# Kernel tuning notes

Hardware: AMD Instinct MI355X
Metric: run time of the kernel (lower is better)

Reference implementation:

```python
import jax, jax.numpy as jnp
import numpy as np

N_IN = 500000
C = 64
K = 27          # kernel volume 3^3
P = 150000      # max pairs per kernel offset
NUM_OUT = 200000


def setup_inputs() -> dict:
    key = jax.random.key(0)
    k1, k2, k3 = jax.random.split(key, 3)
    features = jax.random.normal(k1, (N_IN, C), dtype=jnp.float32)
    # indice_pairs[k, 0, :] = input voxel indices, indice_pairs[k, 1, :] = output voxel indices
    indice_pairs = jax.random.randint(k2, (K, 2, P), 0, NUM_OUT, dtype=jnp.int32)
    indice_pairs_num = jax.random.randint(k3, (K,), 0, P, dtype=jnp.int32)
    return {
        "features": features,
        "indice_pairs": indice_pairs,
        "indice_pairs_num": indice_pairs_num,
        "num_out": NUM_OUT,
    }


def reference(features, indice_pairs, indice_pairs_num, num_out):
    """spconv-style indice_avgpool: gather -> scatter-sum -> divide by count."""
    Kk, _, Pp = indice_pairs.shape
    in_idx = indice_pairs[:, 0, :]   # [K, P]
    out_idx = indice_pairs[:, 1, :]  # [K, P]
    # pairs beyond indice_pairs_num[k] are padding and must be ignored
    valid = jnp.arange(Pp, dtype=jnp.int32)[None, :] < indice_pairs_num[:, None]  # [K, P]
    vmask = valid.astype(features.dtype)
    gathered = features[in_idx.reshape(-1)] * vmask.reshape(-1, 1)               # [K*P, C]
    out_flat = jnp.where(valid, out_idx, 0).reshape(-1)                           # safe scatter target
    out_sum = jnp.zeros((num_out, features.shape[1]), features.dtype).at[out_flat].add(gathered)
    counts = jnp.zeros((num_out,), features.dtype).at[out_flat].add(vmask.reshape(-1))
    return out_sum / jnp.maximum(counts, 1.0)[:, None]
```

## Files before the change

### kernel.cpp

```cpp
#include <hip/hip_runtime.h>

constexpr int N_IN    = 500000;
constexpr int C       = 64;
constexpr int K       = 27;
constexpr int P       = 150000;
constexpr int NUM_OUT = 200000;
constexpr int TOTAL_PAIRS = K * P;
constexpr int OUT_ELEMS   = NUM_OUT * C;

constexpr int OUT_PER_BIN = 128;
constexpr int BIN_SHIFT   = 7;
constexpr int NBINS       = (NUM_OUT + OUT_PER_BIN - 1) / OUT_PER_BIN;

constexpr int PPB        = 16384;
constexpr int PART_BLKS  = (TOTAL_PAIRS + PPB - 1) / PPB;

constexpr int CAP  = 2560;
constexpr int CAPC = 2560;

#define PACK(o_local, in) (((unsigned)(o_local) << 18) | (unsigned)(in))

__global__ void __launch_bounds__(1024)
ap_partition(const int* __restrict__ pairs, const int* __restrict__ nums,
             int* __restrict__ cursor, unsigned int* __restrict__ appendBuf)
{
    __shared__ int binCnt[NBINS];
    __shared__ int binOff[NBINS];
    __shared__ int binDst[NBINS];
    __shared__ int scanTmp[1024];
    __shared__ int snums[K];
    __shared__ unsigned int stage[PPB];
    __shared__ unsigned short sbin[PPB];

    const int tid = threadIdx.x;
    for (int i = tid; i < NBINS; i += 1024) binCnt[i] = 0;
    if (tid < K) snums[tid] = nums[tid];
    __syncthreads();

    const int gbase = blockIdx.x * PPB;

    int4 oc[4];
    int  kk[4];
    int  pp[4];
    int  vv[4];
    #pragma unroll
    for (int j = 0; j < 4; ++j) {
        const int g0 = gbase + (j * 1024 + tid) * 4;
        int v = 0;
        if (g0 < TOTAL_PAIRS) {
            const int k = g0 / P;
            const int p0 = g0 - k * P;
            const int n = snums[k];
            v = n - p0;
            v = v < 0 ? 0 : (v > 4 ? 4 : v);
            kk[j] = k; pp[j] = p0;
            if (v > 0) {
                const int4 o4 = *(const int4*)&pairs[(k * 2 + 1) * P + p0];
                oc[j] = o4;
                atomicAdd(&binCnt[o4.x >> BIN_SHIFT], 1);
                if (v > 1) atomicAdd(&binCnt[o4.y >> BIN_SHIFT], 1);
                if (v > 2) atomicAdd(&binCnt[o4.z >> BIN_SHIFT], 1);
                if (v > 3) atomicAdd(&binCnt[o4.w >> BIN_SHIFT], 1);
            }
        }
        vv[j] = v;
    }
    __syncthreads();

    const int b0 = 2 * tid, b1 = 2 * tid + 1;
    const int c0 = (b0 < NBINS) ? binCnt[b0] : 0;
    const int c1 = (b1 < NBINS) ? binCnt[b1] : 0;
    scanTmp[tid] = c0 + c1;
    __syncthreads();
    for (int d = 1; d < 1024; d <<= 1) {
        int x = (tid >= d) ? scanTmp[tid - d] : 0;
        __syncthreads();
        scanTmp[tid] += x;
        __syncthreads();
    }
    const int Eblk = scanTmp[1023];
    const int ex = scanTmp[tid] - (c0 + c1);
    if (b0 < NBINS) {
        binOff[b0] = ex;
        if (c0 > 0) {
            const int g = atomicAdd(&cursor[b0], c0);
            binDst[b0] = b0 * CAP + g - ex;
        }
        binCnt[b0] = 0;
    }
    if (b1 < NBINS) {
        binOff[b1] = ex + c0;
        if (c1 > 0) {
            const int g = atomicAdd(&cursor[b1], c1);
            binDst[b1] = b1 * CAP + g - (ex + c0);
        }
        binCnt[b1] = 0;
    }
    __syncthreads();

    #pragma unroll
    for (int j = 0; j < 4; ++j) {
        const int v = vv[j];
        if (v > 0) {
            const int4 o4 = oc[j];
            const int4 i4 = *(const int4*)&pairs[(kk[j] * 2) * P + pp[j]];
            {
                const int b = o4.x >> BIN_SHIFT;
                const int pos = binOff[b] + atomicAdd(&binCnt[b], 1);
                stage[pos] = PACK(o4.x & (OUT_PER_BIN - 1), i4.x);
                sbin[pos] = (unsigned short)b;
            }
            if (v > 1) {
                const int b = o4.y >> BIN_SHIFT;
                const int pos = binOff[b] + atomicAdd(&binCnt[b], 1);
                stage[pos] = PACK(o4.y & (OUT_PER_BIN - 1), i4.y);
                sbin[pos] = (unsigned short)b;
            }
            if (v > 2) {
                const int b = o4.z >> BIN_SHIFT;
                const int pos = binOff[b] + atomicAdd(&binCnt[b], 1);
                stage[pos] = PACK(o4.z & (OUT_PER_BIN - 1), i4.z);
                sbin[pos] = (unsigned short)b;
            }
            if (v > 3) {
                const int b = o4.w >> BIN_SHIFT;
                const int pos = binOff[b] + atomicAdd(&binCnt[b], 1);
                stage[pos] = PACK(o4.w & (OUT_PER_BIN - 1), i4.w);
                sbin[pos] = (unsigned short)b;
            }
        }
    }
    __syncthreads();

    for (int e = tid; e < Eblk; e += 1024) {
        const int bb = sbin[e];
        const int d = binDst[bb] + e;
        if (d - bb * CAP < CAP) appendBuf[d] = stage[e];
    }
}

__global__ void __launch_bounds__(256, 4)
ap_bin_reduce(const float* __restrict__ features,
              const unsigned int* __restrict__ appendBuf,
              const int* __restrict__ cursor,
              float* __restrict__ out)
{
    __shared__ int hist[OUT_PER_BIN];
    __shared__ int sc[OUT_PER_BIN];
    __shared__ int cur[OUT_PER_BIN];
    __shared__ unsigned int lb[CAPC];

    const int tid = threadIdx.x;
    const int b = blockIdx.x;
    const int segBase = b * CAP;
    const int Eb = min(cursor[b], CAP);
    const int obase = b * OUT_PER_BIN;

    if (tid < OUT_PER_BIN) hist[tid] = 0;
    __syncthreads();

    uint4 ew[3];
    #pragma unroll
    for (int j = 0; j < 3; ++j) {
        const int e0 = (j * 256 + tid) * 4;
        uint4 w = make_uint4(~0u, ~0u, ~0u, ~0u);
        if (e0 < Eb) {
            w = *(const uint4*)&appendBuf[segBase + e0];
            atomicAdd(&hist[w.x >> 18], 1);
            if (e0 + 1 < Eb) atomicAdd(&hist[w.y >> 18], 1); else w.y = ~0u;
            if (e0 + 2 < Eb) atomicAdd(&hist[w.z >> 18], 1); else w.z = ~0u;
            if (e0 + 3 < Eb) atomicAdd(&hist[w.w >> 18], 1); else w.w = ~0u;
        }
        ew[j] = w;
    }
    __syncthreads();

    int myc = 0;
    if (tid < OUT_PER_BIN) { myc = hist[tid]; sc[tid] = myc; }
    __syncthreads();
    #pragma unroll
    for (int d = 1; d < OUT_PER_BIN; d <<= 1) {
        int x = 0;
        if (tid < OUT_PER_BIN && tid >= d) x = sc[tid - d];
        __syncthreads();
        if (tid < OUT_PER_BIN) sc[tid] += x;
        __syncthreads();
    }
    if (tid < OUT_PER_BIN) cur[tid] = sc[tid] - myc;
    __syncthreads();

    #pragma unroll
    for (int j = 0; j < 3; ++j) {
        const uint4 w = ew[j];
        if (w.x != ~0u) lb[atomicAdd(&cur[w.x >> 18], 1)] = w.x & 0x3FFFFu;
        if (w.y != ~0u) lb[atomicAdd(&cur[w.y >> 18], 1)] = w.y & 0x3FFFFu;
        if (w.z != ~0u) lb[atomicAdd(&cur[w.z >> 18], 1)] = w.z & 0x3FFFFu;
        if (w.w != ~0u) lb[atomicAdd(&cur[w.w >> 18], 1)] = w.w & 0x3FFFFu;
    }
    __syncthreads();

    const int wv   = tid >> 6;
    const int lane = tid & 63;
    const int q    = lane >> 4;
    const int cl   = lane & 15;
    const float* fbase = features + cl * 4;

    for (int r = 0; r < 4; ++r) {
        const int olA = wv * 32 + r * 8 + q;
        const int olB = olA + 4;
        const int oA = obase + olA;
        const int oB = obase + olB;
        const int numA = hist[olA];
        const int numB = hist[olB];
        int sA = min(cur[olA] - numA, CAPC);
        int sB = min(cur[olB] - numB, CAPC);
        const int mA = min(sA + numA, CAPC) - sA;
        const int mB = min(sB + numB, CAPC) - sB;

        float4 a = make_float4(0.f, 0.f, 0.f, 0.f);
        float4 c = make_float4(0.f, 0.f, 0.f, 0.f);
        int eA = 0, eB = 0;

        while (eA + 4 <= mA && eB + 4 <= mB) {
            const int iA0 = (int)lb[sA + eA + 0];
            const int iA1 = (int)lb[sA + eA + 1];
            const int iA2 = (int)lb[sA + eA + 2];
            const int iA3 = (int)lb[sA + eA + 3];
            const int iB0 = (int)lb[sB + eB + 0];
            const int iB1 = (int)lb[sB + eB + 1];
            const int iB2 = (int)lb[sB + eB + 2];
            const int iB3 = (int)lb[sB + eB + 3];
            const float4 vA0 = *(const float4*)&fbase[(size_t)iA0 * C];
            const float4 vA1 = *(const float4*)&fbase[(size_t)iA1 * C];
            const float4 vA2 = *(const float4*)&fbase[(size_t)iA2 * C];
            const float4 vA3 = *(const float4*)&fbase[(size_t)iA3 * C];
            const float4 vB0 = *(const float4*)&fbase[(size_t)iB0 * C];
            const float4 vB1 = *(const float4*)&fbase[(size_t)iB1 * C];
            const float4 vB2 = *(const float4*)&fbase[(size_t)iB2 * C];
            const float4 vB3 = *(const float4*)&fbase[(size_t)iB3 * C];
            a.x += (vA0.x + vA1.x) + (vA2.x + vA3.x);
            a.y += (vA0.y + vA1.y) + (vA2.y + vA3.y);
            a.z += (vA0.z + vA1.z) + (vA2.z + vA3.z);
            a.w += (vA0.w + vA1.w) + (vA2.w + vA3.w);
            c.x += (vB0.x + vB1.x) + (vB2.x + vB3.x);
            c.y += (vB0.y + vB1.y) + (vB2.y + vB3.y);
            c.z += (vB0.z + vB1.z) + (vB2.z + vB3.z);
            c.w += (vB0.w + vB1.w) + (vB2.w + vB3.w);
            eA += 4; eB += 4;
        }
        for (; eA + 4 <= mA; eA += 4) {
            const int i0 = (int)lb[sA + eA + 0];
            const int i1 = (int)lb[sA + eA + 1];
            const int i2 = (int)lb[sA + eA + 2];
            const int i3 = (int)lb[sA + eA + 3];
            const float4 v0 = *(const float4*)&fbase[(size_t)i0 * C];
            const float4 v1 = *(const float4*)&fbase[(size_t)i1 * C];
            const float4 v2 = *(const float4*)&fbase[(size_t)i2 * C];
            const float4 v3 = *(const float4*)&fbase[(size_t)i3 * C];
            a.x += (v0.x + v1.x) + (v2.x + v3.x);
            a.y += (v0.y + v1.y) + (v2.y + v3.y);
            a.z += (v0.z + v1.z) + (v2.z + v3.z);
            a.w += (v0.w + v1.w) + (v2.w + v3.w);
        }
        for (; eA < mA; ++eA) {
            const int i0 = (int)lb[sA + eA];
            const float4 v0 = *(const float4*)&fbase[(size_t)i0 * C];
            a.x += v0.x; a.y += v0.y; a.z += v0.z; a.w += v0.w;
        }
        for (; eB + 4 <= mB; eB += 4) {
            const int i0 = (int)lb[sB + eB + 0];
            const int i1 = (int)lb[sB + eB + 1];
            const int i2 = (int)lb[sB + eB + 2];
            const int i3 = (int)lb[sB + eB + 3];
            const float4 v0 = *(const float4*)&fbase[(size_t)i0 * C];
            const float4 v1 = *(const float4*)&fbase[(size_t)i1 * C];
            const float4 v2 = *(const float4*)&fbase[(size_t)i2 * C];
            const float4 v3 = *(const float4*)&fbase[(size_t)i3 * C];
            c.x += (v0.x + v1.x) + (v2.x + v3.x);
            c.y += (v0.y + v1.y) + (v2.y + v3.y);
            c.z += (v0.z + v1.z) + (v2.z + v3.z);
            c.w += (v0.w + v1.w) + (v2.w + v3.w);
        }
        for (; eB < mB; ++eB) {
            const int i0 = (int)lb[sB + eB];
            const float4 v0 = *(const float4*)&fbase[(size_t)i0 * C];
            c.x += v0.x; c.y += v0.y; c.z += v0.z; c.w += v0.w;
        }

        if (oA < NUM_OUT) {
            const float inv = 1.0f / fmaxf((float)numA, 1.0f);
            a.x *= inv; a.y *= inv; a.z *= inv; a.w *= inv;
            *(float4*)&out[(size_t)oA * C + cl * 4] = a;
        }
        if (oB < NUM_OUT) {
            const float inv = 1.0f / fmaxf((float)numB, 1.0f);
            c.x *= inv; c.y *= inv; c.z *= inv; c.w *= inv;
            *(float4*)&out[(size_t)oB * C + cl * 4] = c;
        }
    }
}

__global__ void __launch_bounds__(256)
sparse_avgpool_scatter(const float* __restrict__ features,
                       const int*   __restrict__ pairs,
                       const int*   __restrict__ nums,
                       float*       __restrict__ out_sum,
                       int*         __restrict__ counts)
{
    const int lane = threadIdx.x & 63;
    const int g = blockIdx.x * (blockDim.x >> 6) + (threadIdx.x >> 6);
    if (g >= TOTAL_PAIRS) return;
    const int k = g / P;
    const int p = g - k * P;
    if (p >= nums[k]) return;
    const int in_idx  = pairs[(k * 2    ) * P + p];
    const int out_idx = pairs[(k * 2 + 1) * P + p];
    const float v = features[(size_t)in_idx * C + lane];
    atomicAdd(&out_sum[(size_t)out_idx * C + lane], v);
    if (lane == 0) atomicAdd(&counts[out_idx], 1);
}

__global__ void __launch_bounds__(256)
sparse_avgpool_divide(float* __restrict__ out, const int* __restrict__ counts)
{
    const int i = blockIdx.x * blockDim.x + threadIdx.x;
    if (i >= OUT_ELEMS) return;
    out[i] /= fmaxf((float)counts[i >> 6], 1.0f);
}

extern "C" void kernel_launch(void* const* d_in, const int* in_sizes, int n_in,
                              void* d_out, int out_size, void* d_ws, size_t ws_size,
                              hipStream_t stream)
{
    const float* features = (const float*)d_in[0];
    const int*   pairs    = (const int*)d_in[1];
    const int*   nums     = (const int*)d_in[2];
    float* out = (float*)d_out;

    const size_t need = (size_t)(2048 + (size_t)NBINS * CAP) * sizeof(int) + 64;

    if (ws_size < need) {
        float* out_sum = out;
        int* counts = (int*)d_ws;
        hipMemsetAsync(out_sum, 0, (size_t)OUT_ELEMS * sizeof(float), stream);
        hipMemsetAsync(counts, 0, (size_t)NUM_OUT * sizeof(int), stream);
        sparse_avgpool_scatter<<<(TOTAL_PAIRS + 3) / 4, 256, 0, stream>>>(
            features, pairs, nums, out, counts);
        sparse_avgpool_divide<<<(OUT_ELEMS + 255) / 256, 256, 0, stream>>>(
            out, counts);
        return;
    }

    int* cursor = (int*)d_ws;
    unsigned int* appendBuf = (unsigned int*)(cursor + 2048);

    hipMemsetAsync(cursor, 0, 2048 * sizeof(int), stream);

    ap_partition<<<PART_BLKS, 1024, 0, stream>>>(pairs, nums, cursor, appendBuf);
    ap_bin_reduce<<<NBINS, 256, 0, stream>>>(features, appendBuf, cursor, out);
}
```

Baseline: 275.4 us.

## Replace per-output counting sort with shared-memory float atomic accumulation in bin reduce

The bin-reduce kernel drops the histogram, prefix scan and counting-sort scatter that grouped pairs by output row. Instead each 16-lane group gathers feature rows straight from the unsorted pair list and adds them with float atomics into a padded shared-memory accumulator of 128 rows by 65 floats. A final pass scales each row by its inverse count and writes it out. This removes several barriers and the scan, but introduces many LDS float atomics with possible contention, about 33KB more LDS per block, and a non-deterministic summation order; the launch-bounds occupancy hint is also removed.

```diff
diff --git a/kernel.cpp b/kernel.cpp
--- a/kernel.cpp
+++ b/kernel.cpp
@@ -17,6 +17,8 @@
 
 constexpr int CAP  = 2560;
 constexpr int CAPC = 2560;
+
+constexpr int ACC_STRIDE = 65;
 
 #define PACK(o_local, in) (((unsigned)(o_local) << 18) | (unsigned)(in))
 
@@ -139,16 +141,18 @@
     }
 }
 
-__global__ void __launch_bounds__(256, 4)
+__global__ void __launch_bounds__(256)
 ap_bin_reduce(const float* __restrict__ features,
               const unsigned int* __restrict__ appendBuf,
               const int* __restrict__ cursor,
               float* __restrict__ out)
 {
-    __shared__ int hist[OUT_PER_BIN];
-    __shared__ int sc[OUT_PER_BIN];
-    __shared__ int cur[OUT_PER_BIN];
-    __shared__ unsigned int lb[CAPC];
+    __shared__ float4 accv[(OUT_PER_BIN * ACC_STRIDE + 3) / 4];
+    __shared__ uint4  lbwv[CAPC / 4];
+    __shared__ int    cnt[OUT_PER_BIN];
+    __shared__ float  inv[OUT_PER_BIN];
+    float*    acc = (float*)accv;
+    unsigned* lbw = (unsigned*)lbwv;
 
     const int tid = threadIdx.x;
     const int b = blockIdx.x;
@@ -156,146 +160,71 @@
     const int Eb = min(cursor[b], CAP);
     const int obase = b * OUT_PER_BIN;
 
-    if (tid < OUT_PER_BIN) hist[tid] = 0;
-    __syncthreads();
-
-    uint4 ew[3];
-    #pragma unroll
-    for (int j = 0; j < 3; ++j) {
-        const int e0 = (j * 256 + tid) * 4;
-        uint4 w = make_uint4(~0u, ~0u, ~0u, ~0u);
-        if (e0 < Eb) {
-            w = *(const uint4*)&appendBuf[segBase + e0];
-            atomicAdd(&hist[w.x >> 18], 1);
-            if (e0 + 1 < Eb) atomicAdd(&hist[w.y >> 18], 1); else w.y = ~0u;
-            if (e0 + 2 < Eb) atomicAdd(&hist[w.z >> 18], 1); else w.z = ~0u;
-            if (e0 + 3 < Eb) atomicAdd(&hist[w.w >> 18], 1); else w.w = ~0u;
-        }
-        ew[j] = w;
-    }
-    __syncthreads();
-
-    int myc = 0;
-    if (tid < OUT_PER_BIN) { myc = hist[tid]; sc[tid] = myc; }
-    __syncthreads();
-    #pragma unroll
-    for (int d = 1; d < OUT_PER_BIN; d <<= 1) {
-        int x = 0;
-        if (tid < OUT_PER_BIN && tid >= d) x = sc[tid - d];
-        __syncthreads();
-        if (tid < OUT_PER_BIN) sc[tid] += x;
-        __syncthreads();
-    }
-    if (tid < OUT_PER_BIN) cur[tid] = sc[tid] - myc;
-    __syncthreads();
-
-    #pragma unroll
-    for (int j = 0; j < 3; ++j) {
-        const uint4 w = ew[j];
-        if (w.x != ~0u) lb[atomicAdd(&cur[w.x >> 18], 1)] = w.x & 0x3FFFFu;
-        if (w.y != ~0u) lb[atomicAdd(&cur[w.y >> 18], 1)] = w.y & 0x3FFFFu;
-        if (w.z != ~0u) lb[atomicAdd(&cur[w.z >> 18], 1)] = w.z & 0x3FFFFu;
-        if (w.w != ~0u) lb[atomicAdd(&cur[w.w >> 18], 1)] = w.w & 0x3FFFFu;
-    }
-    __syncthreads();
-
-    const int wv   = tid >> 6;
-    const int lane = tid & 63;
-    const int q    = lane >> 4;
-    const int cl   = lane & 15;
+    #pragma unroll
+    for (int i = 0; i < (OUT_PER_BIN * ACC_STRIDE + 1023) / 1024; ++i) {
+        const int idx = i * 256 + tid;
+        if (idx < (OUT_PER_BIN * ACC_STRIDE + 3) / 4)
+            accv[idx] = make_float4(0.f, 0.f, 0.f, 0.f);
+    }
+    if (tid < OUT_PER_BIN) cnt[tid] = 0;
+    __syncthreads();
+
+    for (int e0 = tid * 4; e0 < Eb; e0 += 1024) {
+        const uint4 w = *(const uint4*)&appendBuf[segBase + e0];
+        lbwv[e0 >> 2] = w;
+        atomicAdd(&cnt[w.x >> 18], 1);
+        if (e0 + 1 < Eb) atomicAdd(&cnt[w.y >> 18], 1);
+        if (e0 + 2 < Eb) atomicAdd(&cnt[w.z >> 18], 1);
+        if (e0 + 3 < Eb) atomicAdd(&cnt[w.w >> 18], 1);
+    }
+    __syncthreads();
+
+    if (tid < OUT_PER_BIN) inv[tid] = 1.0f / fmaxf((float)cnt[tid], 1.0f);
+
+    const int grp = tid >> 4;
+    const int cl  = tid & 15;
     const float* fbase = features + cl * 4;
 
-    for (int r = 0; r < 4; ++r) {
-        const int olA = wv * 32 + r * 8 + q;
-        const int olB = olA + 4;
-        const int oA = obase + olA;
-        const int oB = obase + olB;
-        const int numA = hist[olA];
-        const int numB = hist[olB];
-        int sA = min(cur[olA] - numA, CAPC);
-        int sB = min(cur[olB] - numB, CAPC);
-        const int mA = min(sA + numA, CAPC) - sA;
-        const int mB = min(sB + numB, CAPC) - sB;
-
-        float4 a = make_float4(0.f, 0.f, 0.f, 0.f);
-        float4 c = make_float4(0.f, 0.f, 0.f, 0.f);
-        int eA = 0, eB = 0;
-
-        while (eA + 4 <= mA && eB + 4 <= mB) {
-            const int iA0 = (int)lb[sA + eA + 0];
-            const int iA1 = (int)lb[sA + eA + 1];
-            const int iA2 = (int)lb[sA + eA + 2];
-            const int iA3 = (int)lb[sA + eA + 3];
-            const int iB0 = (int)lb[sB + eB + 0];
-            const int iB1 = (int)lb[sB + eB + 1];
-            const int iB2 = (int)lb[sB + eB + 2];
-            const int iB3 = (int)lb[sB + eB + 3];
-            const float4 vA0 = *(const float4*)&fbase[(size_t)iA0 * C];
-            const float4 vA1 = *(const float4*)&fbase[(size_t)iA1 * C];
-            const float4 vA2 = *(const float4*)&fbase[(size_t)iA2 * C];
-            const float4 vA3 = *(const float4*)&fbase[(size_t)iA3 * C];
-            const float4 vB0 = *(const float4*)&fbase[(size_t)iB0 * C];
-            const float4 vB1 = *(const float4*)&fbase[(size_t)iB1 * C];
-            const float4 vB2 = *(const float4*)&fbase[(size_t)iB2 * C];
-            const float4 vB3 = *(const float4*)&fbase[(size_t)iB3 * C];
-            a.x += (vA0.x + vA1.x) + (vA2.x + vA3.x);
-            a.y += (vA0.y + vA1.y) + (vA2.y + vA3.y);
-            a.z += (vA0.z + vA1.z) + (vA2.z + vA3.z);
-            a.w += (vA0.w + vA1.w) + (vA2.w + vA3.w);
-            c.x += (vB0.x + vB1.x) + (vB2.x + vB3.x);
-            c.y += (vB0.y + vB1.y) + (vB2.y + vB3.y);
-            c.z += (vB0.z + vB1.z) + (vB2.z + vB3.z);
-            c.w += (vB0.w + vB1.w) + (vB2.w + vB3.w);
-            eA += 4; eB += 4;
-        }
-        for (; eA + 4 <= mA; eA += 4) {
-            const int i0 = (int)lb[sA + eA + 0];
-            const int i1 = (int)lb[sA + eA + 1];
-            const int i2 = (int)lb[sA + eA + 2];
-            const int i3 = (int)lb[sA + eA + 3];
-            const float4 v0 = *(const float4*)&fbase[(size_t)i0 * C];
-            const float4 v1 = *(const float4*)&fbase[(size_t)i1 * C];
-            const float4 v2 = *(const float4*)&fbase[(size_t)i2 * C];
-            const float4 v3 = *(const float4*)&fbase[(size_t)i3 * C];
-            a.x += (v0.x + v1.x) + (v2.x + v3.x);
-            a.y += (v0.y + v1.y) + (v2.y + v3.y);
-            a.z += (v0.z + v1.z) + (v2.z + v3.z);
-            a.w += (v0.w + v1.w) + (v2.w + v3.w);
-        }
-        for (; eA < mA; ++eA) {
-            const int i0 = (int)lb[sA + eA];
-            const float4 v0 = *(const float4*)&fbase[(size_t)i0 * C];
-            a.x += v0.x; a.y += v0.y; a.z += v0.z; a.w += v0.w;
-        }
-        for (; eB + 4 <= mB; eB += 4) {
-            const int i0 = (int)lb[sB + eB + 0];
-            const int i1 = (int)lb[sB + eB + 1];
-            const int i2 = (int)lb[sB + eB + 2];
-            const int i3 = (int)lb[sB + eB + 3];
-            const float4 v0 = *(const float4*)&fbase[(size_t)i0 * C];
-            const float4 v1 = *(const float4*)&fbase[(size_t)i1 * C];
-            const float4 v2 = *(const float4*)&fbase[(size_t)i2 * C];
-            const float4 v3 = *(const float4*)&fbase[(size_t)i3 * C];
-            c.x += (v0.x + v1.x) + (v2.x + v3.x);
-            c.y += (v0.y + v1.y) + (v2.y + v3.y);
-            c.z += (v0.z + v1.z) + (v2.z + v3.z);
-            c.w += (v0.w + v1.w) + (v2.w + v3.w);
-        }
-        for (; eB < mB; ++eB) {
-            const int i0 = (int)lb[sB + eB];
-            const float4 v0 = *(const float4*)&fbase[(size_t)i0 * C];
-            c.x += v0.x; c.y += v0.y; c.z += v0.z; c.w += v0.w;
-        }
-
-        if (oA < NUM_OUT) {
-            const float inv = 1.0f / fmaxf((float)numA, 1.0f);
-            a.x *= inv; a.y *= inv; a.z *= inv; a.w *= inv;
-            *(float4*)&out[(size_t)oA * C + cl * 4] = a;
-        }
-        if (oB < NUM_OUT) {
-            const float inv = 1.0f / fmaxf((float)numB, 1.0f);
-            c.x *= inv; c.y *= inv; c.z *= inv; c.w *= inv;
-            *(float4*)&out[(size_t)oB * C + cl * 4] = c;
+    int e = grp;
+    for (; e + 16 < Eb; e += 32) {
+        const unsigned w0 = lbw[e];
+        const unsigned w1 = lbw[e + 16];
+        const float4 v0 = *(const float4*)&fbase[(size_t)(w0 & 0x3FFFFu) * C];
+        const float4 v1 = *(const float4*)&fbase[(size_t)(w1 & 0x3FFFFu) * C];
+        float* a0 = &acc[(w0 >> 18) * ACC_STRIDE + cl * 4];
+        atomicAdd(a0 + 0, v0.x);
+        atomicAdd(a0 + 1, v0.y);
+        atomicAdd(a0 + 2, v0.z);
+        atomicAdd(a0 + 3, v0.w);
+        float* a1 = &acc[(w1 >> 18) * ACC_STRIDE + cl * 4];
+        atomicAdd(a1 + 0, v1.x);
+        atomicAdd(a1 + 1, v1.y);
+        atomicAdd(a1 + 2, v1.z);
+        atomicAdd(a1 + 3, v1.w);
+    }
+    for (; e < Eb; e += 16) {
+        const unsigned w0 = lbw[e];
+        const float4 v0 = *(const float4*)&fbase[(size_t)(w0 & 0x3FFFFu) * C];
+        float* a0 = &acc[(w0 >> 18) * ACC_STRIDE + cl * 4];
+        atomicAdd(a0 + 0, v0.x);
+        atomicAdd(a0 + 1, v0.y);
+        atomicAdd(a0 + 2, v0.z);
+        atomicAdd(a0 + 3, v0.w);
+    }
+    __syncthreads();
+
+    #pragma unroll
+    for (int i = 0; i < (OUT_PER_BIN * 16) / 256; ++i) {
+        const int idx = i * 256 + tid;
+        const int ol = idx >> 4;
+        const int c4 = (idx & 15) * 4;
+        const int o = obase + ol;
+        if (o < NUM_OUT) {
+            const float s = inv[ol];
+            const float* a = &acc[ol * ACC_STRIDE + c4];
+            float4 r;
+            r.x = a[0] * s; r.y = a[1] * s; r.z = a[2] * s; r.w = a[3] * s;
+            *(float4*)&out[(size_t)o * C + c4] = r;
         }
     }
 }
```

New measurement: 878.1 us. 3.19x slower.

## Split each output bin across two half-bin reduce blocks of 128 threads

Applied to the files above, without the earlier changes.

The bin reduce kernel now launches two 128-thread blocks per 128-output bin. Each block reads the whole bin segment but keeps only the entries whose output falls in its 64-output half. This doubles the number of blocks and halves the shared memory per block, with the aim of better occupancy and load balance across CUs. In exchange every append-buffer segment is read twice, and the local list capacity drops to 1536 entries, which could overflow on skewed bins (overflowing writes are now guarded).

```diff
diff --git a/kernel.cpp b/kernel.cpp
--- a/kernel.cpp
+++ b/kernel.cpp
@@ -16,7 +16,9 @@
 constexpr int PART_BLKS  = (TOTAL_PAIRS + PPB - 1) / PPB;
 
 constexpr int CAP  = 2560;
-constexpr int CAPC = 2560;
+
+constexpr int HOUT   = 64;
+constexpr int CAPC_H = 1536;
 
 #define PACK(o_local, in) (((unsigned)(o_local) << 18) | (unsigned)(in))
 
@@ -139,83 +141,105 @@
     }
 }
 
-__global__ void __launch_bounds__(256, 4)
+__global__ void __launch_bounds__(128, 8)
 ap_bin_reduce(const float* __restrict__ features,
               const unsigned int* __restrict__ appendBuf,
               const int* __restrict__ cursor,
               float* __restrict__ out)
 {
-    __shared__ int hist[OUT_PER_BIN];
-    __shared__ int sc[OUT_PER_BIN];
-    __shared__ int cur[OUT_PER_BIN];
-    __shared__ unsigned int lb[CAPC];
-
-    const int tid = threadIdx.x;
-    const int b = blockIdx.x;
+    __shared__ int hist[HOUT];
+    __shared__ int sc[HOUT];
+    __shared__ int cur[HOUT];
+    __shared__ unsigned int lb[CAPC_H];
+
+    const int tid  = threadIdx.x;
+    const int b    = blockIdx.x >> 1;
+    const int half = blockIdx.x & 1;
     const int segBase = b * CAP;
-    const int Eb = min(cursor[b], CAP);
-    const int obase = b * OUT_PER_BIN;
-
-    if (tid < OUT_PER_BIN) hist[tid] = 0;
-    __syncthreads();
-
-    uint4 ew[3];
-    #pragma unroll
-    for (int j = 0; j < 3; ++j) {
-        const int e0 = (j * 256 + tid) * 4;
+    const int Eb   = min(cursor[b], CAP);
+    const int obase = b * OUT_PER_BIN + half * HOUT;
+
+    if (tid < HOUT) hist[tid] = 0;
+    __syncthreads();
+
+    uint4 ew[5];
+    #pragma unroll
+    for (int j = 0; j < 5; ++j) {
+        const int e0 = (j * 128 + tid) * 4;
         uint4 w = make_uint4(~0u, ~0u, ~0u, ~0u);
         if (e0 < Eb) {
             w = *(const uint4*)&appendBuf[segBase + e0];
-            atomicAdd(&hist[w.x >> 18], 1);
-            if (e0 + 1 < Eb) atomicAdd(&hist[w.y >> 18], 1); else w.y = ~0u;
-            if (e0 + 2 < Eb) atomicAdd(&hist[w.z >> 18], 1); else w.z = ~0u;
-            if (e0 + 3 < Eb) atomicAdd(&hist[w.w >> 18], 1); else w.w = ~0u;
+            if (e0 + 1 >= Eb) w.y = ~0u;
+            if (e0 + 2 >= Eb) w.z = ~0u;
+            if (e0 + 3 >= Eb) w.w = ~0u;
+            if (w.x != ~0u) {
+                if (((w.x >> 24) & 1) == (unsigned)half)
+                    atomicAdd(&hist[(w.x >> 18) & 63], 1);
+                else w.x = ~0u;
+            }
+            if (w.y != ~0u) {
+                if (((w.y >> 24) & 1) == (unsigned)half)
+                    atomicAdd(&hist[(w.y >> 18) & 63], 1);
+                else w.y = ~0u;
+            }
+            if (w.z != ~0u) {
+                if (((w.z >> 24) & 1) == (unsigned)half)
+                    atomicAdd(&hist[(w.z >> 18) & 63], 1);
+                else w.z = ~0u;
+            }
+            if (w.w != ~0u) {
+                if (((w.w >> 24) & 1) == (unsigned)half)
+                    atomicAdd(&hist[(w.w >> 18) & 63], 1);
+                else w.w = ~0u;
+            }
         }
         ew[j] = w;
     }
     __syncthreads();
 
     int myc = 0;
-    if (tid < OUT_PER_BIN) { myc = hist[tid]; sc[tid] = myc; }
-    __syncthreads();
-    #pragma unroll
-    for (int d = 1; d < OUT_PER_BIN; d <<= 1) {
+    if (tid < HOUT) { myc = hist[tid]; sc[tid] = myc; }
+    __syncthreads();
+    #pragma unroll
+    for (int d = 1; d < HOUT; d <<= 1) {
         int x = 0;
-        if (tid < OUT_PER_BIN && tid >= d) x = sc[tid - d];
+        if (tid < HOUT && tid >= d) x = sc[tid - d];
         __syncthreads();
-        if (tid < OUT_PER_BIN) sc[tid] += x;
+        if (tid < HOUT) sc[tid] += x;
         __syncthreads();
     }
-    if (tid < OUT_PER_BIN) cur[tid] = sc[tid] - myc;
-    __syncthreads();
-
-    #pragma unroll
-    for (int j = 0; j < 3; ++j) {
+    if (tid < HOUT) cur[tid] = sc[tid] - myc;
+    __syncthreads();
+
+    #pragma unroll
+    for (int j = 0; j < 5; ++j) {
         const uint4 w = ew[j];
-        if (w.x != ~0u) lb[atomicAdd(&cur[w.x >> 18], 1)] = w.x & 0x3FFFFu;
-        if (w.y != ~0u) lb[atomicAdd(&cur[w.y >> 18], 1)] = w.y & 0x3FFFFu;
-        if (w.z != ~0u) lb[atomicAdd(&cur[w.z >> 18], 1)] = w.z & 0x3FFFFu;
-        if (w.w != ~0u) lb[atomicAdd(&cur[w.w >> 18], 1)] = w.w & 0x3FFFFu;
-    }
-    __syncthreads();
-
-    const int wv   = tid >> 6;
-    const int lane = tid & 63;
-    const int q    = lane >> 4;
-    const int cl   = lane & 15;
+        if (w.x != ~0u) { const int p = atomicAdd(&cur[(w.x >> 18) & 63], 1);
+                          if (p < CAPC_H) lb[p] = w.x & 0x3FFFFu; }
+        if (w.y != ~0u) { const int p = atomicAdd(&cur[(w.y >> 18) & 63], 1);
+                          if (p < CAPC_H) lb[p] = w.y & 0x3FFFFu; }
+        if (w.z != ~0u) { const int p = atomicAdd(&cur[(w.z >> 18) & 63], 1);
+                          if (p < CAPC_H) lb[p] = w.z & 0x3FFFFu; }
+        if (w.w != ~0u) { const int p = atomicAdd(&cur[(w.w >> 18) & 63], 1);
+                          if (p < CAPC_H) lb[p] = w.w & 0x3FFFFu; }
+    }
+    __syncthreads();
+
+    const int qq = tid >> 4;
+    const int cl = tid & 15;
     const float* fbase = features + cl * 4;
 
     for (int r = 0; r < 4; ++r) {
-        const int olA = wv * 32 + r * 8 + q;
+        const int olA = qq * 8 + r;
         const int olB = olA + 4;
         const int oA = obase + olA;
         const int oB = obase + olB;
         const int numA = hist[olA];
         const int numB = hist[olB];
-        int sA = min(cur[olA] - numA, CAPC);
-        int sB = min(cur[olB] - numB, CAPC);
-        const int mA = min(sA + numA, CAPC) - sA;
-        const int mB = min(sB + numB, CAPC) - sB;
+        int sA = min(cur[olA] - numA, CAPC_H);
+        int sB = min(cur[olB] - numB, CAPC_H);
+        const int mA = min(sA + numA, CAPC_H) - sA;
+        const int mB = min(sB + numB, CAPC_H) - sB;
 
         float4 a = make_float4(0.f, 0.f, 0.f, 0.f);
         float4 c = make_float4(0.f, 0.f, 0.f, 0.f);
@@ -357,5 +381,5 @@
     hipMemsetAsync(cursor, 0, 2048 * sizeof(int), stream);
 
     ap_partition<<<PART_BLKS, 1024, 0, stream>>>(pairs, nums, cursor, appendBuf);
-    ap_bin_reduce<<<NBINS, 256, 0, stream>>>(features, appendBuf, cursor, out);
-}
+    ap_bin_reduce<<<NBINS * 2, 128, 0, stream>>>(features, appendBuf, cursor, out);
+}
```

New measurement: 274.2 us (median of 2 runs). No clear change (-0.5%).
